# Kernel tuning notes

Hardware: AMD Instinct MI355X
Metric: run time of the kernel (lower is better)

Reference implementation:

```python
import jax, jax.numpy as jnp
import numpy as np

NEG_SLOPE = 0.2
K_L = 0.5
K_G = 0.5
TEMP_G = 1e-3


def _leaky(v):
    return jnp.where(v >= 0, v, NEG_SLOPE * v)


def _topk_row_mask(scores, keep):
    # scores: [n, n, h]; torch.topk(dim=0) -> indices [keep, n] per head,
    # then head_mask[indices, :] = 1 selects whole ROWS (any column hit).
    n = scores.shape[0]
    s = jnp.transpose(scores, (1, 2, 0))        # [n_cols, h, n_rows]
    _, idx = jax.lax.top_k(s, keep)             # [n_cols, h, keep]

    def per_head(idx_h):                        # idx_h: [n_cols, keep]
        return jnp.zeros((n,), scores.dtype).at[idx_h.reshape(-1)].set(1.0)

    rows = jax.vmap(per_head, in_axes=1, out_axes=0)(idx)  # [h, n_rows]
    return jnp.transpose(rows)[:, None, :]      # [n_rows, 1, h] broadcast over cols


def setup_inputs() -> dict:
    key = jax.random.key(0)
    ks = jax.random.split(key, 8)
    n, in_f, feat_dim = 1024, 256, 128
    H, F = 4, 64                                # n_heads, n_hidden (out_features=256)
    feats = jax.random.normal(ks[0], (n, feat_dim), dtype=jnp.float32)
    x = jax.random.normal(ks[1], (n, in_f), dtype=jnp.float32)
    adj = jax.random.randint(ks[2], (n, n, 1), 0, 2).astype(jnp.int32)
    sc = 0.05
    W_l = jax.random.normal(ks[3], (in_f, H * F), dtype=jnp.float32) * sc
    W_r = jax.random.normal(ks[4], (in_f, H * F), dtype=jnp.float32) * sc
    attn_w = jax.random.normal(ks[5], (F,), dtype=jnp.float32) * sc
    W_delta = jax.random.normal(ks[6], (2 * F, F), dtype=jnp.float32) * sc
    b_delta = jnp.zeros((F,), dtype=jnp.float32)
    return {"feats": feats, "x": x, "adj": adj, "W_l": W_l, "W_r": W_r,
            "attn_w": attn_w, "W_delta": W_delta, "b_delta": b_delta}


def reference(feats, x, adj, W_l, W_r, attn_w, W_delta, b_delta):
    n = x.shape[0]
    F = attn_w.shape[0]
    H = W_l.shape[1] // F
    g_l = (x @ W_l).reshape(n, H, F)
    g_r = (x @ W_r).reshape(n, H, F)
    # g_sum[i, j] = g_l[j] + g_r[i]  (repeat vs repeat_interleave ordering)
    g_sum = g_r[:, None, :, :] + g_l[None, :, :, :]          # [n, n, H, F]
    e = jnp.einsum('ijhf,f->ijh', _leaky(g_sum), attn_w)     # [n, n, H]

    mask_adj = adj > 0                                        # [n, n, 1]
    a_l = jax.nn.softmax(jnp.where(mask_adj, e, -jnp.inf), axis=1)
    a_1nd = a_l * mask_adj.astype(e.dtype)

    keep_l = int(n * (1.0 - K_L))
    a_filt = a_1nd * _topk_row_mask(a_1nd, keep_l)
    attn_local = jnp.einsum('ijh,jhf->ihf', a_filt, g_r)     # [n, H, F]

    omega = jax.nn.softmax(e, axis=1)
    fn = (feats - feats.min(axis=0)) / (feats.max(axis=0) - feats.min(axis=0))
    fn = jnp.where(jnp.isnan(fn), 0.0, fn)
    g_rn = (g_r - g_r.min(axis=0)) / (g_r.max(axis=0) - g_r.min(axis=0))
    nf = jnp.linalg.norm(fn, axis=1)                          # [n] (index j)
    ng = jnp.linalg.norm(g_rn, axis=2)                        # [n, H] (index i)
    alpha = jax.nn.softmax(jnp.abs(nf[None, :, None] - ng[:, None, :]), axis=1)
    gamma = 0.5 * (omega + (1.0 - alpha))

    keep_g = int(n * (1.0 - K_G))
    gf = gamma * _topk_row_mask(gamma, keep_g)
    gf = jax.nn.softmax(jnp.where(gf == 0, 1e-10, gf) / TEMP_G, axis=1)
    attn_global = jnp.einsum('ijh,jhf->ihf', gf, g_r)         # [n, H, F]

    inter = _leaky(jnp.concatenate([attn_local, attn_global], axis=2) @ W_delta + b_delta)
    delta = jax.nn.softmax(inter, axis=1)                     # softmax over heads (torch dim=1)
    attn_res = delta * attn_local + (1.0 - delta) * attn_global
    return attn_res.reshape(n, H * F)
```

## Files before the change

kernel.cpp:

```cpp
#include <hip/hip_runtime.h>
#include <cstdint>
#include <cstddef>

#define N 1024
#define HN 4
#define FDIM 64
#define KSEL 512
#define FLT_MAX_ 3.402823466e+38f

__device__ __forceinline__ float wred_sum(float v){
#pragma unroll
  for(int o=32;o>0;o>>=1) v += __shfl_down(v,o,64);
  return v;
}
__device__ __forceinline__ float bfly_sum(float v){
#pragma unroll
  for(int o=1;o<64;o<<=1) v += __shfl_xor(v,o,64);
  return v;
}
__device__ __forceinline__ float bfly_max(float v){
#pragma unroll
  for(int o=1;o<64;o<<=1) v = fmaxf(v,__shfl_xor(v,o,64));
  return v;
}
__device__ __forceinline__ int bfly_sumi(int v){
#pragma unroll
  for(int o=1;o<64;o<<=1) v += __shfl_xor(v,o,64);
  return v;
}
__device__ __forceinline__ float bred_sum(float v, float* scr){
  int t=threadIdx.x;
  v = wred_sum(v);
  __syncthreads();
  if((t&63)==0) scr[t>>6]=v;
  __syncthreads();
  return (scr[0]+scr[1])+(scr[2]+scr[3]);
}

__global__ __launch_bounds__(256) void pack_adj(const int* __restrict__ adj,
                                                unsigned* __restrict__ adjbit,
                                                int* __restrict__ masks){
  int i = blockIdx.x, t = threadIdx.x, w = t>>6, lane = t&63;
  if(i < 32) masks[i*256 + t] = 0;
#pragma unroll
  for(int it=0; it<4; it++){
    int j = w*256 + it*64 + lane;
    int v = adj[(size_t)i*N + j];
    unsigned long long mb = __ballot(v > 0);
    if(lane == 0){
      adjbit[i*32 + w*8 + it*2]     = (unsigned)mb;
      adjbit[i*32 + w*8 + it*2 + 1] = (unsigned)(mb >> 32);
    }
  }
}

__global__ __launch_bounds__(256) void gemm_lr(const float* __restrict__ x,
                                               const float* __restrict__ W_l,
                                               const float* __restrict__ W_r,
                                               float* __restrict__ g_l,
                                               float* __restrict__ g_r){
  int i0 = blockIdx.x*4, t = threadIdx.x;
  const float* __restrict__ W = blockIdx.y ? W_r : W_l;
  float* __restrict__ g = blockIdx.y ? g_r : g_l;
  float acc[4] = {0.f,0.f,0.f,0.f};
#pragma unroll 8
  for(int k=0;k<256;k++){
    float w = W[(size_t)k*256 + t];
#pragma unroll
    for(int r=0;r<4;r++) acc[r] = fmaf(x[(size_t)(i0+r)*256 + k], w, acc[r]);
  }
#pragma unroll
  for(int r=0;r<4;r++) g[(size_t)(i0+r)*256 + t] = acc[r];
}

__global__ __launch_bounds__(256) void colmm_part(const float* __restrict__ feats,
                                                  const float* __restrict__ g_r,
                                                  float* __restrict__ pmin_f, float* __restrict__ pmax_f,
                                                  float* __restrict__ pmin_g, float* __restrict__ pmax_g){
  int chunk = blockIdx.x, src = blockIdx.y, t = threadIdx.x;
  int cols = src ? 256 : 128;
  const float* in = src ? g_r : feats;
  if(t < cols){
    float lo = FLT_MAX_, hi = -FLT_MAX_;
    int r0 = chunk*64;
    for(int r=0;r<64;r++){
      float v = in[(size_t)(r0+r)*cols + t];
      lo = fminf(lo,v); hi = fmaxf(hi,v);
    }
    if(src){ pmin_g[chunk*256+t]=lo; pmax_g[chunk*256+t]=hi; }
    else   { pmin_f[chunk*128+t]=lo; pmax_f[chunk*128+t]=hi; }
  }
}

__global__ __launch_bounds__(256) void colmm_fin(const float* __restrict__ pmin_f, const float* __restrict__ pmax_f,
                                                 const float* __restrict__ pmin_g, const float* __restrict__ pmax_g,
                                                 float* __restrict__ fmn, float* __restrict__ fmx,
                                                 float* __restrict__ gmn, float* __restrict__ gmx){
  int src = blockIdx.x, t = threadIdx.x;
  int cols = src ? 256 : 128;
  if(t < cols){
    float lo = FLT_MAX_, hi = -FLT_MAX_;
    const float* pn = src ? pmin_g : pmin_f;
    const float* px = src ? pmax_g : pmax_f;
    for(int k=0;k<16;k++){
      lo = fminf(lo, pn[k*cols+t]);
      hi = fmaxf(hi, px[k*cols+t]);
    }
    if(src){ gmn[t]=lo; gmx[t]=hi; } else { fmn[t]=lo; fmx[t]=hi; }
  }
}

__global__ __launch_bounds__(256) void norms_kernel(const float* __restrict__ feats,
                                                    const float* __restrict__ g_r,
                                                    const float* __restrict__ fmn, const float* __restrict__ fmx,
                                                    const float* __restrict__ gmn, const float* __restrict__ gmx,
                                                    float* __restrict__ nf, float* __restrict__ ng){
  __shared__ float scr[4];
  int i = blockIdx.x, z = blockIdx.y, t = threadIdx.x;
  if(z==0){
    float u = 0.f;
    if(t < 128){
      float d = fmx[t]-fmn[t];
      float v = feats[(size_t)i*128 + t];
      u = (d==0.f) ? 0.f : (v - fmn[t])/d;
    }
    float tot = bred_sum(u*u, scr);
    if(t==0) nf[i] = sqrtf(tot);
  } else {
    int c = t, hh = t>>6;
    float d = gmx[c]-gmn[c];
    float v = g_r[(size_t)i*256 + c];
    float u = (v - gmn[c])/d;
    float ss = wred_sum(u*u);
    if((t&63)==0) ng[hh*N + i] = sqrtf(ss);
  }
}

__global__ __launch_bounds__(256) void compute_e(const float* __restrict__ g_l,
                                                 const float* __restrict__ g_r,
                                                 const float* __restrict__ attn_w,
                                                 float* __restrict__ e){
  __shared__ __align__(16) float grs[64][68];
  __shared__ __align__(16) float gls[64][68];
  __shared__ __align__(16) float aw[64], aw2[64];
  int h = blockIdx.z, i0 = blockIdx.y*64, j0 = blockIdx.x*64;
  int t = threadIdx.x;
  if(t < 64){ float w = attn_w[t]; aw[t]=w; aw2[t]=0.2f*w; }
#pragma unroll
  for(int k=0;k<16;k++){
    int idx = t + k*256; int r = idx>>6, f = idx&63;
    grs[r][f] = g_r[(size_t)(i0+r)*256 + h*64 + f];
    gls[r][f] = g_l[(size_t)(j0+r)*256 + h*64 + f];
  }
  __syncthreads();
  int tj = t&15, ti = t>>4;
  float acc[4][4];
#pragma unroll
  for(int a=0;a<4;a++)
#pragma unroll
    for(int b=0;b<4;b++) acc[a][b]=0.f;
  for(int fc=0; fc<64; fc+=4){
    float4 wv  = *(float4*)&aw[fc];
    float4 wv2 = *(float4*)&aw2[fc];
    float4 ga4[4], gb4[4];
#pragma unroll
    for(int a=0;a<4;a++) ga4[a] = *(float4*)&grs[ti*4+a][fc];
#pragma unroll
    for(int b=0;b<4;b++) gb4[b] = *(float4*)&gls[tj+16*b][fc];
#pragma unroll
    for(int a=0;a<4;a++)
#pragma unroll
      for(int b=0;b<4;b++){
        float s0 = ga4[a].x + gb4[b].x;
        float s1 = ga4[a].y + gb4[b].y;
        float s2 = ga4[a].z + gb4[b].z;
        float s3 = ga4[a].w + gb4[b].w;
        acc[a][b] = fmaf(s0, (s0>=0.f)?wv.x:wv2.x, acc[a][b]);
        acc[a][b] = fmaf(s1, (s1>=0.f)?wv.y:wv2.y, acc[a][b]);
        acc[a][b] = fmaf(s2, (s2>=0.f)?wv.z:wv2.z, acc[a][b]);
        acc[a][b] = fmaf(s3, (s3>=0.f)?wv.w:wv2.w, acc[a][b]);
      }
  }
#pragma unroll
  for(int a=0;a<4;a++)
#pragma unroll
    for(int b=0;b<4;b++){
      int i = i0 + ti*4 + a, j = j0 + tj + 16*b;
      e[((size_t)h*N + i)*N + j] = acc[a][b];
    }
}

__global__ __launch_bounds__(256) void row_stats(const float* __restrict__ e,
                                                 const unsigned* __restrict__ adjbit,
                                                 const float* __restrict__ nf,
                                                 const float* __restrict__ ng,
                                                 float* __restrict__ mlA, float* __restrict__ islA,
                                                 float* __restrict__ moA, float* __restrict__ isoA,
                                                 float* __restrict__ maA, float* __restrict__ isaA,
                                                 float* __restrict__ mgA, float* __restrict__ sgA){
  int i = blockIdx.x, t = threadIdx.x, h = t>>6, lane = t&63;
  size_t base = ((size_t)h*N + i)*N;
  float er[16], nfr[16];
  unsigned nib[4];
#pragma unroll
  for(int c=0;c<4;c++){
    float4 e4 = *(const float4*)(e  + base + c*256 + lane*4);
    float4 n4 = *(const float4*)(nf + c*256 + lane*4);
    er[c*4+0]=e4.x; er[c*4+1]=e4.y; er[c*4+2]=e4.z; er[c*4+3]=e4.w;
    nfr[c*4+0]=n4.x; nfr[c*4+1]=n4.y; nfr[c*4+2]=n4.z; nfr[c*4+3]=n4.w;
    nib[c] = (adjbit[i*32 + c*8 + (lane>>3)] >> ((lane&7)*4)) & 0xFu;
  }
  float ngv = ng[h*N + i];
  float ml=-FLT_MAX_, mo=-FLT_MAX_, ma=-FLT_MAX_;
#pragma unroll
  for(int c=0;c<4;c++)
#pragma unroll
    for(int k=0;k<4;k++){
      int q = c*4+k;
      float ev = er[q];
      mo = fmaxf(mo, ev);
      if((nib[c]>>k)&1) ml = fmaxf(ml, ev);
      ma = fmaxf(ma, fabsf(nfr[q]-ngv));
    }
  ml = bfly_max(ml); mo = bfly_max(mo); ma = bfly_max(ma);
  float sl=0.f, so=0.f, sa=0.f;
#pragma unroll
  for(int c=0;c<4;c++)
#pragma unroll
    for(int k=0;k<4;k++){
      int q = c*4+k;
      float ev = er[q];
      so += __expf(ev-mo);
      if((nib[c]>>k)&1) sl += __expf(ev-ml);
      sa += __expf(fabsf(nfr[q]-ngv)-ma);
    }
  sl = bfly_sum(sl); so = bfly_sum(so); sa = bfly_sum(sa);
  float isl = 1.f/sl, iso = 1.f/so, isa = 1.f/sa;
  float gg[16];
  float mg = -FLT_MAX_;
#pragma unroll
  for(int q=0;q<16;q++){
    float ev = er[q];
    float omega = __expf(ev-mo)*iso;
    float alpha = __expf(fabsf(nfr[q]-ngv)-ma)*isa;
    float g = 0.5f*(omega + 1.f - alpha);
    gg[q] = g;
    mg = fmaxf(mg, g);
  }
  mg = bfly_max(mg);
  float sg = 0.f;
#pragma unroll
  for(int q=0;q<16;q++) sg += __expf((gg[q]-mg)/1e-3f);
  sg = bfly_sum(sg);
  if(lane==0){
    mlA[h*N+i]=ml; islA[h*N+i]=isl;
    moA[h*N+i]=mo; isoA[h*N+i]=iso;
    maA[h*N+i]=ma; isaA[h*N+i]=isa;
    mgA[h*N+i]=mg; sgA[h*N+i]=sg;
  }
}

__global__ __launch_bounds__(256) void applyT(float* __restrict__ e,
                                              float* __restrict__ gamT,
                                              const unsigned* __restrict__ adjbit,
                                              const float* __restrict__ nf,
                                              const float* __restrict__ mlA, const float* __restrict__ islA,
                                              const float* __restrict__ moA, const float* __restrict__ isoA,
                                              const float* __restrict__ maA, const float* __restrict__ isaA,
                                              const float* __restrict__ ng){
  __shared__ __align__(16) float buf1[64][65];
  __shared__ __align__(16) float buf2[64][65];
  __shared__ __align__(16) float buf3[64][65];
  __shared__ float rml[64], risl[64], rmo[64], riso[64], rma[64], risa[64], rng[64], nfs[64];
  int h = blockIdx.y;
  int pp = blockIdx.x; int a = 0;
  while(pp >= 16 - a){ pp -= 16 - a; a++; }
  int b = a + pp;
  int t = threadIdx.x;
  int rg = t >> 4, c4 = t & 15;

  int i0 = a*64, j0 = b*64;
  if(t < 64){
    int o = h*N + i0 + t;
    rml[t]=mlA[o]; risl[t]=islA[o]; rmo[t]=moA[o]; riso[t]=isoA[o];
    rma[t]=maA[o]; risa[t]=isaA[o]; rng[t]=ng[o]; nfs[t]=nf[j0+t];
  }
  __syncthreads();
  float4 ev[4]; unsigned nb[4];
#pragma unroll
  for(int k=0;k<4;k++){
    int row = rg*4+k;
    ev[k] = *(const float4*)(e + ((size_t)h*N + i0+row)*N + j0 + c4*4);
    nb[k] = (adjbit[(size_t)(i0+row)*32 + (j0>>5) + (c4>>3)] >> ((c4&7)*4)) & 0xFu;
  }
#pragma unroll
  for(int k=0;k<4;k++){
    int row = rg*4+k;
    float ml=rml[row], isl=risl[row], mo=rmo[row], iso=riso[row];
    float ma=rma[row], isa=risa[row], ngv=rng[row];
    float evc[4] = {ev[k].x,ev[k].y,ev[k].z,ev[k].w};
#pragma unroll
    for(int c=0;c<4;c++){
      int j = c4*4+c;
      buf2[j][row] = ((nb[k]>>c)&1) ? __expf(evc[c]-ml)*isl : 0.f;
      float omega = __expf(evc[c]-mo)*iso;
      float alpha = __expf(fabsf(nfs[j]-ngv)-ma)*isa;
      buf1[j][row] = 0.5f*(omega + 1.f - alpha);
    }
  }
  __syncthreads();
#pragma unroll
  for(int k=0;k<4;k++){
    int jr = rg*4+k;
    *(float4*)(gamT + ((size_t)h*N + j0+jr)*N + i0 + c4*4) = *(float4*)&buf1[jr][c4*4];
  }
  if(a == b){
#pragma unroll
    for(int k=0;k<4;k++){
      int jr = rg*4+k;
      *(float4*)(e + ((size_t)h*N + j0+jr)*N + i0 + c4*4) = *(float4*)&buf2[jr][c4*4];
    }
    return;
  }
  int i1 = b*64, j1 = a*64;
  __syncthreads();
  if(t < 64){
    int o = h*N + i1 + t;
    rml[t]=mlA[o]; risl[t]=islA[o]; rmo[t]=moA[o]; riso[t]=isoA[o];
    rma[t]=maA[o]; risa[t]=isaA[o]; rng[t]=ng[o]; nfs[t]=nf[j1+t];
  }
#pragma unroll
  for(int k=0;k<4;k++){
    int row = rg*4+k;
    ev[k] = *(const float4*)(e + ((size_t)h*N + i1+row)*N + j1 + c4*4);
    nb[k] = (adjbit[(size_t)(i1+row)*32 + (j1>>5) + (c4>>3)] >> ((c4&7)*4)) & 0xFu;
  }
  __syncthreads();
#pragma unroll
  for(int k=0;k<4;k++){
    int jr = rg*4+k;
    *(float4*)(e + ((size_t)h*N + i1+jr)*N + j1 + c4*4) = *(float4*)&buf2[jr][c4*4];
  }
#pragma unroll
  for(int k=0;k<4;k++){
    int row = rg*4+k;
    float ml=rml[row], isl=risl[row], mo=rmo[row], iso=riso[row];
    float ma=rma[row], isa=risa[row], ngv=rng[row];
    float evc[4] = {ev[k].x,ev[k].y,ev[k].z,ev[k].w};
#pragma unroll
    for(int c=0;c<4;c++){
      int j = c4*4+c;
      buf3[j][row] = ((nb[k]>>c)&1) ? __expf(evc[c]-ml)*isl : 0.f;
      float omega = __expf(evc[c]-mo)*iso;
      float alpha = __expf(fabsf(nfs[j]-ngv)-ma)*isa;
      buf1[j][row] = 0.5f*(omega + 1.f - alpha);
    }
  }
  __syncthreads();
#pragma unroll
  for(int k=0;k<4;k++){
    int jr = rg*4+k;
    *(float4*)(gamT + ((size_t)h*N + j1+jr)*N + i1 + c4*4) = *(float4*)&buf1[jr][c4*4];
    *(float4*)(e    + ((size_t)h*N + j1+jr)*N + i1 + c4*4) = *(float4*)&buf3[jr][c4*4];
  }
}

__global__ __launch_bounds__(256) void colselect5(const float* __restrict__ a1T,
                                                  const float* __restrict__ gaT,
                                                  int* __restrict__ mask_l,
                                                  int* __restrict__ mask_g){
  __shared__ __align__(16) int hist[4][256];
  int t = threadIdx.x, w = t>>6, lane = t&63;
  int gcol = blockIdx.x*4 + w;
  int z  = gcol >> 12;
  int hj = gcol & 4095;
  int h  = hj >> 10;
  const float* __restrict__ src = (z ? gaT : a1T) + (size_t)hj * (size_t)N;
  int* __restrict__ mask = z ? mask_g : mask_l;
  int* hw = hist[w];

  unsigned ur[16];
#pragma unroll
  for(int c=0;c<4;c++){
    uint4 u4 = ((const uint4*)src)[c*64 + lane];
    ur[c*4+0]=u4.x; ur[c*4+1]=u4.y; ur[c*4+2]=u4.z; ur[c*4+3]=u4.w;
  }
  unsigned pm = 0;
#pragma unroll
  for(int q=0;q<16;q++) if(ur[q] != 0u) pm |= (1u<<q);
  int cnt_pos = bfly_sumi(__popc(pm));

  unsigned T; int tneed; int tiecnt = -1;
  if(cnt_pos < KSEL){
    T = 0u; tneed = KSEL - cnt_pos;
  } else {
    unsigned am = pm;
    unsigned prefix = 0; int kth = KSEL;
    *(int4*)&hw[lane*4] = make_int4(0,0,0,0);
    {
      unsigned m = am;
      while(m){
        int q = __ffs(m)-1; m &= m-1;
        int bucket = (int)(ur[q] >> 24);
        unsigned long long mb = __ballot(true);
        int lead = __ffsll(mb) - 1;
        int maj = __shfl(bucket, lead, 64);
        if(bucket == maj){
          int cnt = (int)__popcll(__ballot(true));
          if(lane == lead) atomicAdd(&hw[maj], cnt);
        } else atomicAdd(&hw[bucket], 1);
      }
    }
#pragma unroll
    for(int b=3;b>=0;b--){
      if(b < 3){
        *(int4*)&hw[lane*4] = make_int4(0,0,0,0);
        unsigned m = am;
        int shf = 8*(b+1);
        while(m){
          int q = __ffs(m)-1; m &= m-1;
          unsigned u = ur[q];
          if((u >> shf) == prefix){
            int bucket = (int)((u >> (8*b)) & 0xFF);
            unsigned long long mb = __ballot(true);
            int lead = __ffsll(mb) - 1;
            int maj = __shfl(bucket, lead, 64);
            if(bucket == maj){
              int cnt = (int)__popcll(__ballot(true));
              if(lane == lead) atomicAdd(&hw[maj], cnt);
            } else atomicAdd(&hw[bucket], 1);
          } else am &= ~(1u<<q);
        }
      }
      int4 hv = *(int4*)&hw[lane*4];
      int s = hv.x+hv.y+hv.z+hv.w;
      int P = s;
#pragma unroll
      for(int off=1; off<64; off<<=1){
        int q2 = __shfl_up(P, off, 64);
        if(lane >= off) P += q2;
      }
      int total = __shfl(P, 63, 64);
      int suffChunk  = total - (P - s);
      int suffChunkN = total - P;
      bool cross = (suffChunk >= kth) && (suffChunkN < kth);
      int selb=0, newk=0, tcnt=0;
      if(cross){
        int s3 = suffChunkN + hv.w;
        int s2 = s3 + hv.z;
        int s1 = s2 + hv.y;
        if(s3 >= kth){ selb=4*lane+3; newk = kth - suffChunkN; tcnt=hv.w; }
        else if(s2 >= kth){ selb=4*lane+2; newk = kth - s3; tcnt=hv.z; }
        else if(s1 >= kth){ selb=4*lane+1; newk = kth - s2; tcnt=hv.y; }
        else { selb=4*lane; newk = kth - s1; tcnt=hv.x; }
      }
      unsigned long long cm = __ballot(cross);
      int csrc = __ffsll(cm) - 1;
      selb   = __shfl(selb, csrc, 64);
      kth    = __shfl(newk, csrc, 64);
      tiecnt = __shfl(tcnt, csrc, 64);
      prefix = (prefix << 8) | (unsigned)selb;
    }
    T = prefix; tneed = kth;
  }

  if(tiecnt == tneed){
#pragma unroll
    for(int c=0;c<4;c++)
#pragma unroll
      for(int k2=0;k2<4;k2++){
        int i = c*256 + lane*4 + k2;
        if(ur[c*4+k2] >= T) mask[h*N + i] = 1;
      }
  } else {
    int base = 0;
#pragma unroll
    for(int c=0;c<4;c++){
      int tc=0;
#pragma unroll
      for(int k2=0;k2<4;k2++) tc += (ur[c*4+k2]==T)?1:0;
      int pc = tc;
#pragma unroll
      for(int off=1; off<64; off<<=1){
        int q2 = __shfl_up(pc, off, 64);
        if(lane >= off) pc += q2;
      }
      int ctot = __shfl(pc, 63, 64);
      int run = base + pc - tc;
#pragma unroll
      for(int k2=0;k2<4;k2++){
        int i = c*256 + lane*4 + k2;
        unsigned u = ur[c*4+k2];
        bool sel = (u > T) || (u == T && run < tneed);
        run += (u==T)?1:0;
        if(sel) mask[h*N + i] = 1;
      }
      base += ctot;
    }
  }
}

__global__ __launch_bounds__(256) void attn_mm(const float* __restrict__ a1T,
                                               const float* __restrict__ gaT,
                                               const float* __restrict__ g_r,
                                               const float* __restrict__ mgA,
                                               const float* __restrict__ sgA,
                                               const int* __restrict__ mask_g,
                                               float* __restrict__ partL,
                                               float* __restrict__ partG){
  __shared__ __align__(16) float a_t[32][68];
  __shared__ __align__(16) float p_t[32][68];
  __shared__ __align__(16) float b_s[32][68];
  __shared__ float mgv[64], isgv[64];
  __shared__ int mgf[64];
  int i0 = blockIdx.x*64, h = blockIdx.y, s = blockIdx.z, j0 = s*128;
  int t = threadIdx.x;
  if(t < 64){
    mgv[t]  = mgA[h*N + i0 + t];
    isgv[t] = 1.f / sgA[h*N + i0 + t];
    mgf[t]  = mask_g[h*N + i0 + t];
  }
  __syncthreads();
  int fq = t & 15, iq = t >> 4;
  float4 accL[4], accG[4];
#pragma unroll
  for(int r=0;r<4;r++){ accL[r]=make_float4(0,0,0,0); accG[r]=make_float4(0,0,0,0); }
  for(int sub=0; sub<4; sub++){
    int jb = j0 + sub*32;
#pragma unroll
    for(int k=0;k<2;k++){
      int idx = t + k*256;
      int jj = idx>>4, i4 = idx&15;
      size_t base = ((size_t)h*N + jb + jj)*N + i0 + i4*4;
      *(float4*)&a_t[jj][i4*4] = *(const float4*)(a1T + base);
      float4 g4 = *(const float4*)(gaT + base);
      int ii = i4*4;
      const float inv = 1.f/1024.f;
      float4 p4;
      p4.x = mgf[ii+0] ? __expf((g4.x - mgv[ii+0])/1e-3f)*isgv[ii+0] : inv;
      p4.y = mgf[ii+1] ? __expf((g4.y - mgv[ii+1])/1e-3f)*isgv[ii+1] : inv;
      p4.z = mgf[ii+2] ? __expf((g4.z - mgv[ii+2])/1e-3f)*isgv[ii+2] : inv;
      p4.w = mgf[ii+3] ? __expf((g4.w - mgv[ii+3])/1e-3f)*isgv[ii+3] : inv;
      *(float4*)&p_t[jj][i4*4] = p4;
      *(float4*)&b_s[jj][i4*4] = *(const float4*)(g_r + (size_t)(jb+jj)*256 + h*64 + i4*4);
    }
    __syncthreads();
#pragma unroll 4
    for(int j=0;j<32;j++){
      float4 bv = *(float4*)&b_s[j][fq*4];
      float4 av = *(float4*)&a_t[j][iq*4];
      float4 pv = *(float4*)&p_t[j][iq*4];
      accL[0].x = fmaf(av.x, bv.x, accL[0].x); accL[0].y = fmaf(av.x, bv.y, accL[0].y);
      accL[0].z = fmaf(av.x, bv.z, accL[0].z); accL[0].w = fmaf(av.x, bv.w, accL[0].w);
      accL[1].x = fmaf(av.y, bv.x, accL[1].x); accL[1].y = fmaf(av.y, bv.y, accL[1].y);
      accL[1].z = fmaf(av.y, bv.z, accL[1].z); accL[1].w = fmaf(av.y, bv.w, accL[1].w);
      accL[2].x = fmaf(av.z, bv.x, accL[2].x); accL[2].y = fmaf(av.z, bv.y, accL[2].y);
      accL[2].z = fmaf(av.z, bv.z, accL[2].z); accL[2].w = fmaf(av.z, bv.w, accL[2].w);
      accL[3].x = fmaf(av.w, bv.x, accL[3].x); accL[3].y = fmaf(av.w, bv.y, accL[3].y);
      accL[3].z = fmaf(av.w, bv.z, accL[3].z); accL[3].w = fmaf(av.w, bv.w, accL[3].w);
      accG[0].x = fmaf(pv.x, bv.x, accG[0].x); accG[0].y = fmaf(pv.x, bv.y, accG[0].y);
      accG[0].z = fmaf(pv.x, bv.z, accG[0].z); accG[0].w = fmaf(pv.x, bv.w, accG[0].w);
      accG[1].x = fmaf(pv.y, bv.x, accG[1].x); accG[1].y = fmaf(pv.y, bv.y, accG[1].y);
      accG[1].z = fmaf(pv.y, bv.z, accG[1].z); accG[1].w = fmaf(pv.y, bv.w, accG[1].w);
      accG[2].x = fmaf(pv.z, bv.x, accG[2].x); accG[2].y = fmaf(pv.z, bv.y, accG[2].y);
      accG[2].z = fmaf(pv.z, bv.z, accG[2].z); accG[2].w = fmaf(pv.z, bv.w, accG[2].w);
      accG[3].x = fmaf(pv.w, bv.x, accG[3].x); accG[3].y = fmaf(pv.w, bv.y, accG[3].y);
      accG[3].z = fmaf(pv.w, bv.z, accG[3].z); accG[3].w = fmaf(pv.w, bv.w, accG[3].w);
    }
    __syncthreads();
  }
#pragma unroll
  for(int r=0;r<4;r++){
    int i = i0 + iq*4 + r;
    size_t o = ((size_t)s*N + i)*256 + h*64 + fq*4;
    *(float4*)&partL[o] = accL[r];
    *(float4*)&partG[o] = accG[r];
  }
}

__global__ __launch_bounds__(256) void epilogue(const float* __restrict__ partL,
                                                const float* __restrict__ partG,
                                                const int* __restrict__ mask_l,
                                                const float* __restrict__ W_delta,
                                                const float* __restrict__ b_delta,
                                                float* __restrict__ out){
  __shared__ float cat[4][128];
  __shared__ float inter_s[4][64];
  int i = blockIdx.x, t = threadIdx.x;
  int h = t>>6, f = t&63;
  float sl = 0.f, sg = 0.f;
#pragma unroll
  for(int s2=0;s2<8;s2++){
    size_t o = ((size_t)s2*N + i)*256 + h*64 + f;
    sl += partL[o];
    sg += partG[o];
  }
  if(!mask_l[h*N + i]) sl = 0.f;
  cat[h][f]      = sl;
  cat[h][64 + f] = sg;
  __syncthreads();
  float d = b_delta[f];
  for(int c=0;c<128;c++) d = fmaf(cat[h][c], W_delta[(size_t)c*64 + f], d);
  d = (d >= 0.f) ? d : 0.2f*d;
  inter_s[h][f] = d;
  __syncthreads();
  float m = inter_s[0][f];
#pragma unroll
  for(int hh=1;hh<4;hh++) m = fmaxf(m, inter_s[hh][f]);
  float ssum = 0.f;
#pragma unroll
  for(int hh=0;hh<4;hh++) ssum += __expf(inter_s[hh][f]-m);
  float delta = __expf(d - m)/ssum;
  out[(size_t)i*256 + h*64 + f] = delta*sl + (1.f - delta)*sg;
}

extern "C" void kernel_launch(void* const* d_in, const int* in_sizes, int n_in,
                              void* d_out, int out_size, void* d_ws, size_t ws_size,
                              hipStream_t stream) {
  const float* feats  = (const float*)d_in[0];
  const float* x      = (const float*)d_in[1];
  const int*   adj    = (const int*)  d_in[2];
  const float* W_l    = (const float*)d_in[3];
  const float* W_r    = (const float*)d_in[4];
  const float* attn_w = (const float*)d_in[5];
  const float* W_delta= (const float*)d_in[6];
  const float* b_delta= (const float*)d_in[7];
  float* out = (float*)d_out;

  float* ws = (float*)d_ws;
  size_t off = 0;
  float* g_l   = ws+off; off += (size_t)N*256;
  float* g_r   = ws+off; off += (size_t)N*256;
  float* e     = ws+off; off += (size_t)HN*N*N;
  float* gam   = ws+off; off += (size_t)HN*N*N;
  float* partL = ws+off; off += (size_t)8*N*256;
  float* partG = ws+off; off += (size_t)8*N*256;
  float* pmin_f= ws+off; off += 16*128;
  float* pmax_f= ws+off; off += 16*128;
  float* pmin_g= ws+off; off += 16*256;
  float* pmax_g= ws+off; off += 16*256;
  float* fmn   = ws+off; off += 128;
  float* fmx   = ws+off; off += 128;
  float* gmn   = ws+off; off += 256;
  float* gmx   = ws+off; off += 256;
  float* nf    = ws+off; off += N;
  float* ng    = ws+off; off += (size_t)HN*N;
  float* mlA   = ws+off; off += (size_t)HN*N;
  float* islA  = ws+off; off += (size_t)HN*N;
  float* moA   = ws+off; off += (size_t)HN*N;
  float* isoA  = ws+off; off += (size_t)HN*N;
  float* maA   = ws+off; off += (size_t)HN*N;
  float* isaA  = ws+off; off += (size_t)HN*N;
  float* mgA   = ws+off; off += (size_t)HN*N;
  float* sgA   = ws+off; off += (size_t)HN*N;
  int* mask_l  = (int*)(ws+off); off += (size_t)HN*N;
  int* mask_g  = (int*)(ws+off); off += (size_t)HN*N;
  unsigned* adjbit = (unsigned*)(ws+off); off += (size_t)N*32;

  pack_adj<<<N, 256, 0, stream>>>(adj, adjbit, mask_l);

  gemm_lr<<<dim3(256,2), 256, 0, stream>>>(x, W_l, W_r, g_l, g_r);

  colmm_part<<<dim3(16,2), 256, 0, stream>>>(feats, g_r, pmin_f, pmax_f, pmin_g, pmax_g);
  colmm_fin <<<dim3(2),    256, 0, stream>>>(pmin_f, pmax_f, pmin_g, pmax_g, fmn, fmx, gmn, gmx);
  norms_kernel<<<dim3(N,2),256, 0, stream>>>(feats, g_r, fmn, fmx, gmn, gmx, nf, ng);

  compute_e<<<dim3(16,16,HN), 256, 0, stream>>>(g_l, g_r, attn_w, e);

  row_stats<<<N, 256, 0, stream>>>(e, adjbit, nf, ng, mlA, islA, moA, isoA, maA, isaA, mgA, sgA);

  applyT<<<dim3(136,HN), 256, 0, stream>>>(e, gam, adjbit, nf, mlA, islA, moA, isoA, maA, isaA, ng);

  colselect5<<<2048, 256, 0, stream>>>(e, gam, mask_l, mask_g);

  attn_mm<<<dim3(16,HN,8), 256, 0, stream>>>(e, gam, g_r, mgA, sgA, mask_g, partL, partG);

  epilogue<<<N, 256, 0, stream>>>(partL, partG, mask_l, W_delta, b_delta, out);
}
```

Before: 219.8 us.

## Merge small prologue kernels, simplify radix-select histogram, halve attn_mm row tile

```diff
diff --git a/kernel.cpp b/kernel.cpp
--- a/kernel.cpp
+++ b/kernel.cpp
@@ -37,47 +37,51 @@
   return (scr[0]+scr[1])+(scr[2]+scr[3]);
 }
 
-__global__ __launch_bounds__(256) void pack_adj(const int* __restrict__ adj,
-                                                unsigned* __restrict__ adjbit,
-                                                int* __restrict__ masks){
-  int i = blockIdx.x, t = threadIdx.x, w = t>>6, lane = t&63;
-  if(i < 32) masks[i*256 + t] = 0;
-#pragma unroll
-  for(int it=0; it<4; it++){
-    int j = w*256 + it*64 + lane;
-    int v = adj[(size_t)i*N + j];
-    unsigned long long mb = __ballot(v > 0);
-    if(lane == 0){
-      adjbit[i*32 + w*8 + it*2]     = (unsigned)mb;
-      adjbit[i*32 + w*8 + it*2 + 1] = (unsigned)(mb >> 32);
-    }
-  }
-}
-
-__global__ __launch_bounds__(256) void gemm_lr(const float* __restrict__ x,
-                                               const float* __restrict__ W_l,
-                                               const float* __restrict__ W_r,
-                                               float* __restrict__ g_l,
-                                               float* __restrict__ g_r){
-  int i0 = blockIdx.x*4, t = threadIdx.x;
-  const float* __restrict__ W = blockIdx.y ? W_r : W_l;
-  float* __restrict__ g = blockIdx.y ? g_r : g_l;
-  float acc[4] = {0.f,0.f,0.f,0.f};
+__global__ __launch_bounds__(256) void stage1(const float* __restrict__ x,
+                                              const float* __restrict__ W_l,
+                                              const float* __restrict__ W_r,
+                                              const int* __restrict__ adj,
+                                              float* __restrict__ g_l,
+                                              float* __restrict__ g_r,
+                                              unsigned* __restrict__ adjbit,
+                                              int* __restrict__ masks){
+  int bx = blockIdx.x, t = threadIdx.x;
+  if(bx < 512){
+    const float* __restrict__ W = (bx >= 256) ? W_r : W_l;
+    float* __restrict__ g = (bx >= 256) ? g_r : g_l;
+    int i0 = (bx & 255)*4;
+    float acc[4] = {0.f,0.f,0.f,0.f};
 #pragma unroll 8
-  for(int k=0;k<256;k++){
-    float w = W[(size_t)k*256 + t];
-#pragma unroll
-    for(int r=0;r<4;r++) acc[r] = fmaf(x[(size_t)(i0+r)*256 + k], w, acc[r]);
-  }
-#pragma unroll
-  for(int r=0;r<4;r++) g[(size_t)(i0+r)*256 + t] = acc[r];
+    for(int k=0;k<256;k++){
+      float w = W[(size_t)k*256 + t];
+#pragma unroll
+      for(int r=0;r<4;r++) acc[r] = fmaf(x[(size_t)(i0+r)*256 + k], w, acc[r]);
+    }
+#pragma unroll
+    for(int r=0;r<4;r++) g[(size_t)(i0+r)*256 + t] = acc[r];
+  } else {
+    int i = bx - 512, w = t>>6, lane = t&63;
+    if(i < 32) masks[i*256 + t] = 0;
+#pragma unroll
+    for(int it=0; it<4; it++){
+      int j = w*256 + it*64 + lane;
+      int v = adj[(size_t)i*N + j];
+      unsigned long long mb = __ballot(v > 0);
+      if(lane == 0){
+        adjbit[i*32 + w*8 + it*2]     = (unsigned)mb;
+        adjbit[i*32 + w*8 + it*2 + 1] = (unsigned)(mb >> 32);
+      }
+    }
+  }
 }
 
 __global__ __launch_bounds__(256) void colmm_part(const float* __restrict__ feats,
                                                   const float* __restrict__ g_r,
                                                   float* __restrict__ pmin_f, float* __restrict__ pmax_f,
                                                   float* __restrict__ pmin_g, float* __restrict__ pmax_g){
-  int chunk = blockIdx.x, src = blockIdx.y, t = threadIdx.x;
+  int bx = blockIdx.x, t = threadIdx.x;
+  int src = (bx >= 16) ? 1 : 0;
+  int chunk = src ? bx-16 : bx;
   int cols = src ? 256 : 128;
   const float* in = src ? g_r : feats;
   if(t < cols){
@@ -92,45 +96,39 @@
   }
 }
 
-__global__ __launch_bounds__(256) void colmm_fin(const float* __restrict__ pmin_f, const float* __restrict__ pmax_f,
-                                                 const float* __restrict__ pmin_g, const float* __restrict__ pmax_g,
-                                                 float* __restrict__ fmn, float* __restrict__ fmx,
-                                                 float* __restrict__ gmn, float* __restrict__ gmx){
-  int src = blockIdx.x, t = threadIdx.x;
-  int cols = src ? 256 : 128;
-  if(t < cols){
-    float lo = FLT_MAX_, hi = -FLT_MAX_;
-    const float* pn = src ? pmin_g : pmin_f;
-    const float* px = src ? pmax_g : pmax_f;
-    for(int k=0;k<16;k++){
-      lo = fminf(lo, pn[k*cols+t]);
-      hi = fmaxf(hi, px[k*cols+t]);
-    }
-    if(src){ gmn[t]=lo; gmx[t]=hi; } else { fmn[t]=lo; fmx[t]=hi; }
-  }
-}
-
 __global__ __launch_bounds__(256) void norms_kernel(const float* __restrict__ feats,
                                                     const float* __restrict__ g_r,
-                                                    const float* __restrict__ fmn, const float* __restrict__ fmx,
-                                                    const float* __restrict__ gmn, const float* __restrict__ gmx,
+                                                    const float* __restrict__ pmin_f, const float* __restrict__ pmax_f,
+                                                    const float* __restrict__ pmin_g, const float* __restrict__ pmax_g,
                                                     float* __restrict__ nf, float* __restrict__ ng){
   __shared__ float scr[4];
   int i = blockIdx.x, z = blockIdx.y, t = threadIdx.x;
   if(z==0){
     float u = 0.f;
     if(t < 128){
-      float d = fmx[t]-fmn[t];
+      float lo = FLT_MAX_, hi = -FLT_MAX_;
+#pragma unroll
+      for(int k=0;k<16;k++){
+        lo = fminf(lo, pmin_f[k*128+t]);
+        hi = fmaxf(hi, pmax_f[k*128+t]);
+      }
+      float d = hi - lo;
       float v = feats[(size_t)i*128 + t];
-      u = (d==0.f) ? 0.f : (v - fmn[t])/d;
+      u = (d==0.f) ? 0.f : (v - lo)/d;
     }
     float tot = bred_sum(u*u, scr);
     if(t==0) nf[i] = sqrtf(tot);
   } else {
     int c = t, hh = t>>6;
-    float d = gmx[c]-gmn[c];
+    float lo = FLT_MAX_, hi = -FLT_MAX_;
+#pragma unroll
+    for(int k=0;k<16;k++){
+      lo = fminf(lo, pmin_g[k*256+c]);
+      hi = fmaxf(hi, pmax_g[k*256+c]);
+    }
+    float d = hi - lo;
     float v = g_r[(size_t)i*256 + c];
-    float u = (v - gmn[c])/d;
+    float u = (v - lo)/d;
     float ss = wred_sum(u*u);
     if((t&63)==0) ng[hh*N + i] = sqrtf(ss);
   }
@@ -365,7 +363,7 @@
   }
 }
 
-__global__ __launch_bounds__(256) void colselect5(const float* __restrict__ a1T,
+__global__ __launch_bounds__(256) void colselect6(const float* __restrict__ a1T,
                                                   const float* __restrict__ gaT,
                                                   int* __restrict__ mask_l,
                                                   int* __restrict__ mask_g){
@@ -385,51 +383,34 @@
     uint4 u4 = ((const uint4*)src)[c*64 + lane];
     ur[c*4+0]=u4.x; ur[c*4+1]=u4.y; ur[c*4+2]=u4.z; ur[c*4+3]=u4.w;
   }
-  unsigned pm = 0;
-#pragma unroll
-  for(int q=0;q<16;q++) if(ur[q] != 0u) pm |= (1u<<q);
-  int cnt_pos = bfly_sumi(__popc(pm));
+  int np = 0;
+#pragma unroll
+  for(int q=0;q<16;q++) np += (ur[q] != 0u) ? 1 : 0;
+  int cnt_pos = bfly_sumi(np);
 
   unsigned T; int tneed; int tiecnt = -1;
   if(cnt_pos < KSEL){
     T = 0u; tneed = KSEL - cnt_pos;
   } else {
-    unsigned am = pm;
     unsigned prefix = 0; int kth = KSEL;
-    *(int4*)&hw[lane*4] = make_int4(0,0,0,0);
-    {
-      unsigned m = am;
-      while(m){
-        int q = __ffs(m)-1; m &= m-1;
-        int bucket = (int)(ur[q] >> 24);
-        unsigned long long mb = __ballot(true);
-        int lead = __ffsll(mb) - 1;
-        int maj = __shfl(bucket, lead, 64);
-        if(bucket == maj){
-          int cnt = (int)__popcll(__ballot(true));
-          if(lane == lead) atomicAdd(&hw[maj], cnt);
-        } else atomicAdd(&hw[bucket], 1);
-      }
-    }
 #pragma unroll
     for(int b=3;b>=0;b--){
-      if(b < 3){
-        *(int4*)&hw[lane*4] = make_int4(0,0,0,0);
-        unsigned m = am;
-        int shf = 8*(b+1);
-        while(m){
-          int q = __ffs(m)-1; m &= m-1;
-          unsigned u = ur[q];
-          if((u >> shf) == prefix){
-            int bucket = (int)((u >> (8*b)) & 0xFF);
-            unsigned long long mb = __ballot(true);
-            int lead = __ffsll(mb) - 1;
-            int maj = __shfl(bucket, lead, 64);
-            if(bucket == maj){
-              int cnt = (int)__popcll(__ballot(true));
-              if(lane == lead) atomicAdd(&hw[maj], cnt);
-            } else atomicAdd(&hw[bucket], 1);
-          } else am &= ~(1u<<q);
+      *(int4*)&hw[lane*4] = make_int4(0,0,0,0);
+#pragma unroll
+      for(int q=0;q<16;q++){
+        unsigned u = ur[q];
+        bool act = (b==3) || ((u >> (8*(b+1))) == prefix);
+        if(act){
+          int bucket = (u >> (8*b)) & 0xFF;
+          unsigned long long mball = __ballot(true);
+          int lead = __ffsll(mball) - 1;
+          int maj = __shfl(bucket, lead, 64);
+          if(bucket == maj){
+            int cnt = (int)__popcll(__ballot(true));
+            if(lane == lead) atomicAdd(&hw[maj], cnt);
+          } else {
+            atomicAdd(&hw[bucket], 1);
+          }
         }
       }
       int4 hv = *(int4*)&hw[lane*4];
@@ -508,29 +489,27 @@
                                                const int* __restrict__ mask_g,
                                                float* __restrict__ partL,
                                                float* __restrict__ partG){
-  __shared__ __align__(16) float a_t[32][68];
-  __shared__ __align__(16) float p_t[32][68];
+  __shared__ __align__(16) float a_t[32][36];
+  __shared__ __align__(16) float p_t[32][36];
   __shared__ __align__(16) float b_s[32][68];
-  __shared__ float mgv[64], isgv[64];
-  __shared__ int mgf[64];
-  int i0 = blockIdx.x*64, h = blockIdx.y, s = blockIdx.z, j0 = s*128;
+  __shared__ float mgv[32], isgv[32];
+  __shared__ int mgf[32];
+  int i0 = blockIdx.x*32, h = blockIdx.y, s = blockIdx.z, j0 = s*128;
   int t = threadIdx.x;
-  if(t < 64){
+  if(t < 32){
     mgv[t]  = mgA[h*N + i0 + t];
     isgv[t] = 1.f / sgA[h*N + i0 + t];
     mgf[t]  = mask_g[h*N + i0 + t];
   }
   __syncthreads();
   int fq = t & 15, iq = t >> 4;
-  float4 accL[4], accG[4];
-#pragma unroll
-  for(int r=0;r<4;r++){ accL[r]=make_float4(0,0,0,0); accG[r]=make_float4(0,0,0,0); }
+  float4 accL[2], accG[2];
+#pragma unroll
+  for(int r=0;r<2;r++){ accL[r]=make_float4(0,0,0,0); accG[r]=make_float4(0,0,0,0); }
   for(int sub=0; sub<4; sub++){
     int jb = j0 + sub*32;
-#pragma unroll
-    for(int k=0;k<2;k++){
-      int idx = t + k*256;
-      int jj = idx>>4, i4 = idx&15;
+    {
+      int jj = t>>3, i4 = t&7;
       size_t base = ((size_t)h*N + jb + jj)*N + i0 + i4*4;
       *(float4*)&a_t[jj][i4*4] = *(const float4*)(a1T + base);
       float4 g4 = *(const float4*)(gaT + base);
@@ -542,36 +521,33 @@
       p4.z = mgf[ii+2] ? __expf((g4.z - mgv[ii+2])/1e-3f)*isgv[ii+2] : inv;
       p4.w = mgf[ii+3] ? __expf((g4.w - mgv[ii+3])/1e-3f)*isgv[ii+3] : inv;
       *(float4*)&p_t[jj][i4*4] = p4;
-      *(float4*)&b_s[jj][i4*4] = *(const float4*)(g_r + (size_t)(jb+jj)*256 + h*64 + i4*4);
+#pragma unroll
+      for(int k=0;k<2;k++){
+        int idx = t + k*256;
+        int jb2 = idx>>4, d4 = idx&15;
+        *(float4*)&b_s[jb2][d4*4] = *(const float4*)(g_r + (size_t)(jb+jb2)*256 + h*64 + d4*4);
+      }
     }
     __syncthreads();
-#pragma unroll 4
+#pragma unroll 8
     for(int j=0;j<32;j++){
       float4 bv = *(float4*)&b_s[j][fq*4];
-      float4 av = *(float4*)&a_t[j][iq*4];
-      float4 pv = *(float4*)&p_t[j][iq*4];
+      float2 av = *(float2*)&a_t[j][iq*2];
+      float2 pv = *(float2*)&p_t[j][iq*2];
       accL[0].x = fmaf(av.x, bv.x, accL[0].x); accL[0].y = fmaf(av.x, bv.y, accL[0].y);
       accL[0].z = fmaf(av.x, bv.z, accL[0].z); accL[0].w = fmaf(av.x, bv.w, accL[0].w);
       accL[1].x = fmaf(av.y, bv.x, accL[1].x); accL[1].y = fmaf(av.y, bv.y, accL[1].y);
       accL[1].z = fmaf(av.y, bv.z, accL[1].z); accL[1].w = fmaf(av.y, bv.w, accL[1].w);
-      accL[2].x = fmaf(av.z, bv.x, accL[2].x); accL[2].y = fmaf(av.z, bv.y, accL[2].y);
-      accL[2].z = fmaf(av.z, bv.z, accL[2].z); accL[2].w = fmaf(av.z, bv.w, accL[2].w);
-      accL[3].x = fmaf(av.w, bv.x, accL[3].x); accL[3].y = fmaf(av.w, bv.y, accL[3].y);
-      accL[3].z = fmaf(av.w, bv.z, accL[3].z); accL[3].w = fmaf(av.w, bv.w, accL[3].w);
       accG[0].x = fmaf(pv.x, bv.x, accG[0].x); accG[0].y = fmaf(pv.x, bv.y, accG[0].y);
       accG[0].z = fmaf(pv.x, bv.z, accG[0].z); accG[0].w = fmaf(pv.x, bv.w, accG[0].w);
       accG[1].x = fmaf(pv.y, bv.x, accG[1].x); accG[1].y = fmaf(pv.y, bv.y, accG[1].y);
       accG[1].z = fmaf(pv.y, bv.z, accG[1].z); accG[1].w = fmaf(pv.y, bv.w, accG[1].w);
-      accG[2].x = fmaf(pv.z, bv.x, accG[2].x); accG[2].y = fmaf(pv.z, bv.y, accG[2].y);
-      accG[2].z = fmaf(pv.z, bv.z, accG[2].z); accG[2].w = fmaf(pv.z, bv.w, accG[2].w);
-      accG[3].x = fmaf(pv.w, bv.x, accG[3].x); accG[3].y = fmaf(pv.w, bv.y, accG[3].y);
-      accG[3].z = fmaf(pv.w, bv.z, accG[3].z); accG[3].w = fmaf(pv.w, bv.w, accG[3].w);
     }
     __syncthreads();
   }
 #pragma unroll
-  for(int r=0;r<4;r++){
-    int i = i0 + iq*4 + r;
+  for(int r=0;r<2;r++){
+    int i = i0 + iq*2 + r;
     size_t o = ((size_t)s*N + i)*256 + h*64 + fq*4;
     *(float4*)&partL[o] = accL[r];
     *(float4*)&partG[o] = accG[r];
@@ -639,10 +615,6 @@
   float* pmax_f= ws+off; off += 16*128;
   float* pmin_g= ws+off; off += 16*256;
   float* pmax_g= ws+off; off += 16*256;
-  float* fmn   = ws+off; off += 128;
-  float* fmx   = ws+off; off += 128;
-  float* gmn   = ws+off; off += 256;
-  float* gmx   = ws+off; off += 256;
   float* nf    = ws+off; off += N;
   float* ng    = ws+off; off += (size_t)HN*N;
   float* mlA   = ws+off; off += (size_t)HN*N;
@@ -657,13 +629,11 @@
   int* mask_g  = (int*)(ws+off); off += (size_t)HN*N;
   unsigned* adjbit = (unsigned*)(ws+off); off += (size_t)N*32;
 
-  pack_adj<<<N, 256, 0, stream>>>(adj, adjbit, mask_l);
-
-  gemm_lr<<<dim3(256,2), 256, 0, stream>>>(x, W_l, W_r, g_l, g_r);
-
-  colmm_part<<<dim3(16,2), 256, 0, stream>>>(feats, g_r, pmin_f, pmax_f, pmin_g, pmax_g);
-  colmm_fin <<<dim3(2),    256, 0, stream>>>(pmin_f, pmax_f, pmin_g, pmax_g, fmn, fmx, gmn, gmx);
-  norms_kernel<<<dim3(N,2),256, 0, stream>>>(feats, g_r, fmn, fmx, gmn, gmx, nf, ng);
+  stage1<<<1536, 256, 0, stream>>>(x, W_l, W_r, adj, g_l, g_r, adjbit, mask_l);
+
+  colmm_part<<<32, 256, 0, stream>>>(feats, g_r, pmin_f, pmax_f, pmin_g, pmax_g);
+
+  norms_kernel<<<dim3(N,2), 256, 0, stream>>>(feats, g_r, pmin_f, pmax_f, pmin_g, pmax_g, nf, ng);
 
   compute_e<<<dim3(16,16,HN), 256, 0, stream>>>(g_l, g_r, attn_w, e);
 
@@ -671,9 +641,9 @@
 
   applyT<<<dim3(136,HN), 256, 0, stream>>>(e, gam, adjbit, nf, mlA, islA, moA, isoA, maA, isaA, ng);
 
-  colselect5<<<2048, 256, 0, stream>>>(e, gam, mask_l, mask_g);
-
-  attn_mm<<<dim3(16,HN,8), 256, 0, stream>>>(e, gam, g_r, mgA, sgA, mask_g, partL, partG);
+  colselect6<<<2048, 256, 0, stream>>>(e, gam, mask_l, mask_g);
+
+  attn_mm<<<dim3(32,HN,8), 256, 0, stream>>>(e, gam, g_r, mgA, sgA, mask_g, partL, partG);
 
   epilogue<<<N, 256, 0, stream>>>(partL, partG, mask_l, W_delta, b_delta, out);
 }
```

Result: faster. 203.6 us (-7.4%).
